# Kernel tuning notes

Measured on AMD Instinct MI355X. Metric: run time of the kernel, lower is better.

## Reference

```python
import jax, jax.numpy as jnp
import numpy as np

N = 100000   # nodes
E = 1600000  # edges
IN_DIM, HID, HEADS, OUT_DIM = 8, 64, 4, 3


def _add_self_loops(src, dst, n):
    loop = jnp.arange(n, dtype=src.dtype)
    return jnp.concatenate([src, loop]), jnp.concatenate([dst, loop])


def gcn_conv(x, src, dst, n, W, b):
    # PyG GCNConv: add self-loops, symmetric normalization deg^-1/2 * deg^-1/2
    s, d = _add_self_loops(src, dst, n)
    deg = jax.ops.segment_sum(jnp.ones(s.shape[0], x.dtype), d, num_segments=n)
    dinv = jnp.where(deg > 0, jax.lax.rsqrt(deg), 0.0)
    norm = dinv[s] * dinv[d]                       # [E']
    h = x @ W                                      # [N, out]
    out = jax.ops.segment_sum(norm[:, None] * h[s], d, num_segments=n)
    return out + b


def gat_conv(x, src, dst, n, W, att_src, att_dst, b):
    # PyG GATConv, concat=True, negative_slope=0.2, self-loops added
    h = (x @ W).reshape(n, HEADS, HID)             # [N, H, C]
    s, d = _add_self_loops(src, dst, n)
    a_src = jnp.sum(h * att_src, axis=-1)          # [N, H]
    a_dst = jnp.sum(h * att_dst, axis=-1)          # [N, H]
    e = jax.nn.leaky_relu(a_src[s] + a_dst[d], negative_slope=0.2)  # [E', H]
    m = jax.lax.stop_gradient(jax.ops.segment_max(e, d, num_segments=n))
    ex = jnp.exp(e - m[d])
    denom = jax.ops.segment_sum(ex, d, num_segments=n)
    alpha = ex / (denom[d] + 1e-16)                # segment softmax over incoming edges
    out = jax.ops.segment_sum(alpha[:, :, None] * h[s], d, num_segments=n)  # [N, H, C]
    return out.reshape(n, HEADS * HID) + b


def setup_inputs() -> dict:
    key = jax.random.key(0)
    ks = jax.random.split(key, 16)
    def glorot(k, shape):
        fan = shape[0] + shape[-1]
        return jax.random.normal(k, shape, jnp.float32) * np.sqrt(2.0 / fan)
    return {
        "x": jax.random.normal(ks[0], (N, IN_DIM), jnp.float32),
        "edge_index": jax.random.randint(ks[1], (2, E), 0, N, jnp.int64 if jax.config.jax_enable_x64 else jnp.int32),
        "w1": glorot(ks[2], (IN_DIM, HID)), "b1": jnp.zeros((HID,), jnp.float32),
        "w2": glorot(ks[3], (HID, HID)),   "b2": jnp.zeros((HID,), jnp.float32),
        "w3": glorot(ks[4], (HID, HID)),   "b3": jnp.zeros((HID,), jnp.float32),
        "wg": glorot(ks[5], (HID, HEADS * HID)), "bg": jnp.zeros((HEADS * HID,), jnp.float32),
        "att_src": glorot(ks[6], (HEADS, HID)),
        "att_dst": glorot(ks[7], (HEADS, HID)),
        "wc1": glorot(ks[8], (HEADS * HID, HID)), "bc1": jnp.zeros((HID,), jnp.float32),
        "wc2": glorot(ks[9], (HID, OUT_DIM)),     "bc2": jnp.zeros((OUT_DIM,), jnp.float32),
    }


def reference(x, edge_index, w1, b1, w2, b2, w3, b3, wg, bg, att_src, att_dst, wc1, bc1, wc2, bc2):
    src, dst = edge_index[0], edge_index[1]
    n = x.shape[0]
    # stacked GCN convs with ReLU; residual when shapes match (layers 2,3)
    h = jax.nn.relu(gcn_conv(x, src, dst, n, w1, b1))
    h = h + jax.nn.relu(gcn_conv(h, src, dst, n, w2, b2))
    h = h + jax.nn.relu(gcn_conv(h, src, dst, n, w3, b3))
    # GAT attention layer (4 heads, concat)
    h_att = gat_conv(h, src, dst, n, wg, att_src, att_dst, bg)  # [N, 256]
    # classifier MLP (dropout is inference no-op)
    z = jax.nn.relu(h_att @ wc1 + bc1)
    logits = z @ wc2 + bc2
    return jax.nn.log_softmax(logits, axis=1)
```

## Files before the change

### kernel.cpp

```cpp
#include <hip/hip_runtime.h>
#include <math.h>


typedef _Float16 half8 __attribute__((ext_vector_type(8)));
typedef _Float16 f16x8 __attribute__((ext_vector_type(8)));
typedef float f32x4 __attribute__((ext_vector_type(4)));

__device__ __forceinline__ float leaky02(float v) { return v > 0.f ? v : 0.2f * v; }


template <int CTRL>
__device__ __forceinline__ float dpp_add(float v) {
    int iv = __builtin_bit_cast(int, v);
    int r = __builtin_amdgcn_update_dpp(iv, iv, CTRL, 0xF, 0xF, false);
    return v + __builtin_bit_cast(float, r);
}
template <int OFF>
__device__ __forceinline__ float swz_add(float v) {
    int r = __builtin_amdgcn_ds_swizzle(__builtin_bit_cast(int, v), OFF);
    return v + __builtin_bit_cast(float, r);
}
__device__ __forceinline__ float red8(float v) {
    v = dpp_add<0xB1>(v);
    v = dpp_add<0x4E>(v);
    v = swz_add<0x101F>(v);
    return v;
}
__device__ __forceinline__ float red16(float v) {
    v = dpp_add<0xB1>(v);
    v = dpp_add<0x4E>(v);
    v = swz_add<0x101F>(v);
    v = dpp_add<0x128>(v);
    return v;
}
__device__ __forceinline__ float red64(float v) {
    v = dpp_add<0xB1>(v);
    v = dpp_add<0x4E>(v);
    v = swz_add<0x101F>(v);
    v = dpp_add<0x128>(v);
    v = swz_add<0x401F>(v);
    v = v + __shfl_xor(v, 32);
    return v;
}
__device__ __forceinline__ float sel4(int g, float v0, float v1, float v2, float v3) {
    return g == 0 ? v0 : g == 1 ? v1 : g == 2 ? v2 : v3;
}


__global__ void count_kernel(const int* __restrict__ dst, int E, int range,
                             int* __restrict__ counts) {
    int grp = blockIdx.x & 7;
    int nlo = grp * range;
    int nhi = nlo + range;
    int nblk = gridDim.x >> 3;
    int c = blockIdx.x >> 3;
    int stride = nblk * blockDim.x;
    for (int e = c * blockDim.x + threadIdx.x; e < E; e += stride) {
        int d = dst[e];
        if (d >= nlo && d < nhi) atomicAdd(&counts[d], 1);
    }
}

__global__ void scan_pass1(const int* __restrict__ counts, int n, int* __restrict__ blockSums) {
    __shared__ int sh[256];
    int base = blockIdx.x * 2048;
    int tid = threadIdx.x;
    int s = 0;
#pragma unroll
    for (int j = 0; j < 8; ++j) {
        int idx = base + tid * 8 + j;
        if (idx < n) s += counts[idx];
    }
    sh[tid] = s;
    __syncthreads();
    for (int off = 128; off > 0; off >>= 1) {
        if (tid < off) sh[tid] += sh[tid + off];
        __syncthreads();
    }
    if (tid == 0) blockSums[blockIdx.x] = sh[0];
}

__global__ void scan_pass2(const int* __restrict__ blockSums, int nb, int* __restrict__ blockOffs) {
    if (threadIdx.x == 0 && blockIdx.x == 0) {
        int run = 0;
        for (int i = 0; i < nb; ++i) { blockOffs[i] = run; run += blockSums[i]; }
    }
}

__global__ void scan_pass3(const int* __restrict__ counts, int n,
                           const int* __restrict__ blockOffs,
                           const float* __restrict__ x,
                           int* __restrict__ row_ptr, int* __restrict__ cursor,
                           float* __restrict__ dinv, float* __restrict__ rdinv,
                           _Float16* __restrict__ xs) {
    __shared__ int sh[256];
    int base = blockIdx.x * 2048;
    int tid = threadIdx.x;
    int cnt[8];
    int local = 0;
#pragma unroll
    for (int j = 0; j < 8; ++j) {
        int idx = base + tid * 8 + j;
        cnt[j] = (idx < n) ? counts[idx] : 0;
        local += cnt[j];
    }
    sh[tid] = local;
    __syncthreads();
    for (int off = 1; off < 256; off <<= 1) {
        int v = (tid >= off) ? sh[tid - off] : 0;
        __syncthreads();
        sh[tid] += v;
        __syncthreads();
    }
    int run = blockOffs[blockIdx.x] + sh[tid] - local;
#pragma unroll
    for (int j = 0; j < 8; ++j) {
        int idx = base + tid * 8 + j;
        if (idx < n) {
            row_ptr[idx] = run;
            cursor[idx] = run;
            float dv = rsqrtf((float)(cnt[j] + 1));
            dinv[idx] = dv;
            rdinv[idx] = sqrtf((float)(cnt[j] + 1));
#pragma unroll
            for (int t = 0; t < 8; ++t) xs[idx * 8 + t] = (_Float16)(dv * x[idx * 8 + t]);
            run += cnt[j];
            if (idx == n - 1) row_ptr[n] = run;
        }
    }
}

__global__ void scatter_kernel(const int* __restrict__ src, const int* __restrict__ dst,
                               int E, int range,
                               int* __restrict__ cursor, int* __restrict__ col_src) {
    int grp = blockIdx.x & 7;
    int nlo = grp * range;
    int nhi = nlo + range;
    int nblk = gridDim.x >> 3;
    int c = blockIdx.x >> 3;
    int stride = nblk * blockDim.x;
    for (int e = c * blockDim.x + threadIdx.x; e < E; e += stride) {
        int d = dst[e];
        if (d >= nlo && d < nhi) {
            int pos = atomicAdd(&cursor[d], 1);
            col_src[pos] = src[e];
        }
    }
}


__global__ void ccomb_kernel(const float* __restrict__ Wg, const float* __restrict__ bg,
                             const float* __restrict__ wc1, const float* __restrict__ bc1,
                             const float* __restrict__ att_src, const float* __restrict__ att_dst,
                             _Float16* __restrict__ CcombP, float* __restrict__ bcomb,
                             float* __restrict__ wse, float* __restrict__ wde) {
    int bid = blockIdx.x;
    int j = threadIdx.x;
    if (bid < 256) {
        int i = bid;
        float s = 0.f;
        for (int c = 0; c < 64; ++c)
            s += Wg[(i & 63) * 256 + (i >> 6) * 64 + c] * wc1[((i >> 6) * 64 + c) * 64 + j];
        _Float16 hi = (_Float16)s;
        _Float16 lo = (_Float16)(s - (float)hi);
        int kt = i >> 5, l = (((i >> 3) & 3) << 4) | (j & 15), e = i & 7, ct = j >> 4;
        CcombP[(ct * 8 + kt) * 512 + l * 8 + e] = hi;
        CcombP[(32 + ct * 8 + kt) * 512 + l * 8 + e] = lo;
    } else {
        float s = bc1[j];
        for (int i = 0; i < 256; ++i) s += bg[i] * wc1[i * 64 + j];
        bcomb[j] = s;
#pragma unroll
        for (int h = 0; h < 4; ++h) {
            float ss = 0.f, sd = 0.f;
            for (int c = 0; c < 64; ++c) {
                float w = Wg[j * 256 + h * 64 + c];
                ss += w * att_src[h * 64 + c];
                sd += w * att_dst[h * 64 + c];
            }
            wse[j * 4 + h] = ss;
            wde[j * 4 + h] = sd;
        }
    }
}


__global__ void gcn_layer1(const half8* __restrict__ xs8,
                           const float* __restrict__ W1, const float* __restrict__ b1,
                           const int* __restrict__ row_ptr, const int* __restrict__ col_src,
                           const float* __restrict__ dinv, int n,
                           _Float16* __restrict__ hs1) {
    int tid = threadIdx.x, lane = tid & 63, wid = tid >> 6;
    int node = blockIdx.x * 4 + wid;
    if (node >= n) return;
    int beg = row_ptr[node], end = row_ptr[node + 1];
    int deg = end - beg;
    float acc[8] = {0.f, 0.f, 0.f, 0.f, 0.f, 0.f, 0.f, 0.f};
    for (int base = 0; base < deg; base += 64) {
        int cs = col_src[min(beg + base + lane, end - 1)];
        half8 v = xs8[cs];
        if (base + lane < deg) {
#pragma unroll
            for (int c = 0; c < 8; ++c) acc[c] += (float)v[c];
        }
    }
#pragma unroll
    for (int c = 0; c < 8; ++c) acc[c] = red64(acc[c]);
    half8 sv = xs8[node];
    float di = dinv[node];
    float agg[8];
#pragma unroll
    for (int c = 0; c < 8; ++c) agg[c] = (acc[c] + (float)sv[c]) * di;
    float sum = b1[lane];
#pragma unroll
    for (int k = 0; k < 8; ++k) sum = fmaf(agg[k], W1[k * 64 + lane], sum);
    hs1[node * 64 + lane] = (_Float16)(di * fmaxf(sum, 0.f));
}


template <bool LAST>
__global__ void gcn_layer64(const _Float16* __restrict__ hs_in,
                            const float* __restrict__ W, const float* __restrict__ b,
                            const int* __restrict__ row_ptr, const int* __restrict__ col_src,
                            const float* __restrict__ dinv, const float* __restrict__ rdinv,
                            const float* __restrict__ wse, const float* __restrict__ wde,
                            int n,
                            _Float16* __restrict__ hout,
                            float4* __restrict__ a_src4, float4* __restrict__ a_dst4) {
    __shared__ float agg_lds[4][64];
    int tid = threadIdx.x;
    int lane = tid & 63;
    int wid = tid >> 6;
    int t = lane >> 3, g = lane & 7;
    const half8* hs8 = (const half8*)hs_in;
    float wreg[64];
#pragma unroll
    for (int k = 0; k < 64; ++k) wreg[k] = W[k * 64 + lane];
    float bl = b[lane];
    float4 we, wd;
    if (LAST) {
        we = ((const float4*)wse)[lane];
        wd = ((const float4*)wde)[lane];
    }
    int nw = gridDim.x * 4;
    for (int node = blockIdx.x * 4 + wid; node < n; node += nw) {
        int beg = row_ptr[node], end = row_ptr[node + 1];
        int deg = end - beg;
        half8 sv = hs8[node * 8 + t];
        float ac[8];
#pragma unroll
        for (int c = 0; c < 8; ++c) ac[c] = (g == 0) ? (float)sv[c] : 0.f;
        for (int base = 0; base < deg; base += 64) {
            int cs = col_src[min(beg + base + lane, end - 1)];
            int lim = min(deg - base, 64);
            auto bodyF = [&](int eo8) {
                int s = __shfl(cs, eo8 + g);
                half8 v = hs8[s * 8 + t];
#pragma unroll
                for (int c = 0; c < 8; ++c) ac[c] += (float)v[c];
            };
            auto bodyG = [&](int eo8) {
                int eo = eo8 + g;
                int s = __shfl(cs, eo);
                half8 v = hs8[s * 8 + t];
                if (eo < lim) {
#pragma unroll
                    for (int c = 0; c < 8; ++c) ac[c] += (float)v[c];
                }
            };
            int eo8 = 0;
            for (; eo8 + 16 <= lim; eo8 += 16) { bodyF(eo8); bodyF(eo8 + 8); }
            if (eo8 < lim) {
                bodyG(eo8);
                eo8 += 8;
                if (eo8 < lim) bodyG(eo8);
            }
        }
        float di = dinv[node];
#pragma unroll
        for (int c = 0; c < 8; ++c) ac[c] = red8(ac[c]) * di;
        if (g == 0) {
            *(float4*)&agg_lds[wid][t * 8]     = make_float4(ac[0], ac[1], ac[2], ac[3]);
            *(float4*)&agg_lds[wid][t * 8 + 4] = make_float4(ac[4], ac[5], ac[6], ac[7]);
        }
        __asm__ volatile("s_waitcnt lgkmcnt(0)" ::: "memory");
        float sum = bl;
#pragma unroll
        for (int k4 = 0; k4 < 16; ++k4) {
            float4 a4 = *(const float4*)&agg_lds[wid][k4 * 4];
            sum = fmaf(a4.x, wreg[k4 * 4 + 0], sum);
            sum = fmaf(a4.y, wreg[k4 * 4 + 1], sum);
            sum = fmaf(a4.z, wreg[k4 * 4 + 2], sum);
            sum = fmaf(a4.w, wreg[k4 * 4 + 3], sum);
        }
        float hprev = rdinv[node] * (float)sv[g];
        float hv = hprev + fmaxf(sum, 0.f);
        if (!LAST) {
            hout[node * 64 + lane] = (_Float16)(di * hv);
        } else {
            hout[node * 64 + lane] = (_Float16)hv;
            float vs0 = red64(hv * we.x), vs1 = red64(hv * we.y);
            float vs2 = red64(hv * we.z), vs3 = red64(hv * we.w);
            float vd0 = red64(hv * wd.x), vd1 = red64(hv * wd.y);
            float vd2 = red64(hv * wd.z), vd3 = red64(hv * wd.w);
            if (lane == 0) {
                a_src4[node] = make_float4(vs0, vs1, vs2, vs3);
                a_dst4[node] = make_float4(vd0, vd1, vd2, vd3);
            }
        }
    }
}


__global__ void gat_agg(const _Float16* __restrict__ h3,
                        const float4* __restrict__ a_src4, const float4* __restrict__ a_dst4,
                        const int* __restrict__ row_ptr, const int* __restrict__ col_src,
                        int n, _Float16* __restrict__ aggout) {
    __shared__ float4 w_lds[4][64];
    __shared__ int    s_lds[4][64];
    int tid = threadIdx.x, lane = tid & 63, wid = tid >> 6;
    int node = blockIdx.x * 4 + wid;
    if (node >= n) return;
    int t = lane >> 3, g = lane & 7;
    const half8* h38 = (const half8*)h3;

    float4 ad = a_dst4[node];
    half8 hself = h38[node * 8 + t];
    float A[4][8], dh[4];
    {
        float4 asf = a_src4[node];
        float w0 = __expf(leaky02(asf.x + ad.x));
        float w1 = __expf(leaky02(asf.y + ad.y));
        float w2 = __expf(leaky02(asf.z + ad.z));
        float w3 = __expf(leaky02(asf.w + ad.w));
        float m0 = (g == 0) ? 1.f : 0.f;
        dh[0] = m0 * w0; dh[1] = m0 * w1; dh[2] = m0 * w2; dh[3] = m0 * w3;
#pragma unroll
        for (int c = 0; c < 8; ++c) {
            float hvc = (float)hself[c];
            A[0][c] = dh[0] * hvc;
            A[1][c] = dh[1] * hvc;
            A[2][c] = dh[2] * hvc;
            A[3][c] = dh[3] * hvc;
        }
    }
    int beg = row_ptr[node], end = row_ptr[node + 1];
    int deg = end - beg;
    for (int base = 0; base < deg; base += 64) {
        int cs = col_src[min(beg + base + lane, end - 1)];
        float4 as = a_src4[cs];
        float valid = (base + lane < deg) ? 1.f : 0.f;
        float4 wv;
        wv.x = valid * __expf(leaky02(as.x + ad.x));
        wv.y = valid * __expf(leaky02(as.y + ad.y));
        wv.z = valid * __expf(leaky02(as.z + ad.z));
        wv.w = valid * __expf(leaky02(as.w + ad.w));
        w_lds[wid][lane] = wv;
        s_lds[wid][lane] = cs;
        __asm__ volatile("s_waitcnt lgkmcnt(0)" ::: "memory");
        int lim = min(deg - base, 64);
        auto body = [&](int eo8) {
            int eo = eo8 + g;
            int s = s_lds[wid][eo];
            float4 w4 = w_lds[wid][eo];
            half8 hv = h38[s * 8 + t];
#pragma unroll
            for (int c = 0; c < 8; ++c) {
                float hvc = (float)hv[c];
                A[0][c] = fmaf(w4.x, hvc, A[0][c]);
                A[1][c] = fmaf(w4.y, hvc, A[1][c]);
                A[2][c] = fmaf(w4.z, hvc, A[2][c]);
                A[3][c] = fmaf(w4.w, hvc, A[3][c]);
            }
            dh[0] += w4.x; dh[1] += w4.y; dh[2] += w4.z; dh[3] += w4.w;
        };
        int eo8 = 0;
        for (; eo8 + 16 <= lim; eo8 += 16) { body(eo8); body(eo8 + 8); }
        if (eo8 < lim) {
            body(eo8);
            eo8 += 8;
            if (eo8 < lim) body(eo8);
        }
    }
#pragma unroll
    for (int h = 0; h < 4; ++h) {
#pragma unroll
        for (int c = 0; c < 8; ++c) A[h][c] = red8(A[h][c]);
        dh[h] = red8(dh[h]);
    }
    float r0 = 1.f / (dh[0] + 1e-16f);
    float r1 = 1.f / (dh[1] + 1e-16f);
    float r2 = 1.f / (dh[2] + 1e-16f);
    float r3 = 1.f / (dh[3] + 1e-16f);
    if (g < 4) {
        float r = sel4(g, r0, r1, r2, r3);
        half8 hv;
#pragma unroll
        for (int c = 0; c < 8; ++c)
            hv[c] = (_Float16)(sel4(g, A[0][c], A[1][c], A[2][c], A[3][c]) * r);
        *(half8*)(aggout + (size_t)node * 256 + g * 64 + t * 8) = hv;
    }
}


__global__ __launch_bounds__(256) void mlp_mfma(
        const _Float16* __restrict__ agg,
        const _Float16* __restrict__ CP,
        const float* __restrict__ bcomb,
        const float* __restrict__ wc2, const float* __restrict__ bc2,
        int n, float* __restrict__ out) {
    __shared__ float part[4][16][3];
    int tid = threadIdx.x;
    int lane = tid & 63;
    int w = __builtin_amdgcn_readfirstlane(tid >> 6);
    int c16 = lane & 15, hi = lane >> 4;

    f16x8 bh[8], blo[8];
#pragma unroll
    for (int kt = 0; kt < 8; ++kt) {
        bh[kt]  = *(const f16x8*)(CP + (size_t)(w * 8 + kt) * 512 + lane * 8);
        blo[kt] = *(const f16x8*)(CP + (size_t)(32 + w * 8 + kt) * 512 + lane * 8);
    }
    int col = w * 16 + c16;
    float bc  = bcomb[col];
    float w20 = wc2[col * 3 + 0], w21 = wc2[col * 3 + 1], w22 = wc2[col * 3 + 2];
    float bb0 = bc2[0], bb1 = bc2[1], bb2 = bc2[2];

    int ntiles = (n + 15) >> 4;
    for (int tile = blockIdx.x; tile < ntiles; tile += gridDim.x) {
        int rowb = tile * 16;
        int row = min(rowb + c16, n - 1);
        const _Float16* ap = agg + (size_t)row * 256 + hi * 8;
        f16x8 a[8];
#pragma unroll
        for (int kt = 0; kt < 8; ++kt) a[kt] = *(const f16x8*)(ap + kt * 32);
        f32x4 acc = {0.f, 0.f, 0.f, 0.f};
#pragma unroll
        for (int kt = 0; kt < 8; ++kt) {
            acc = __builtin_amdgcn_mfma_f32_16x16x32_f16(a[kt], bh[kt],  acc, 0, 0, 0);
            acc = __builtin_amdgcn_mfma_f32_16x16x32_f16(a[kt], blo[kt], acc, 0, 0, 0);
        }
        float pr[4][3];
#pragma unroll
        for (int r = 0; r < 4; ++r) {
            float z = fmaxf(acc[r] + bc, 0.f);
            pr[r][0] = red16(z * w20);
            pr[r][1] = red16(z * w21);
            pr[r][2] = red16(z * w22);
        }
        if (c16 == 0) {
#pragma unroll
            for (int r = 0; r < 4; ++r) {
                part[w][hi * 4 + r][0] = pr[r][0];
                part[w][hi * 4 + r][1] = pr[r][1];
                part[w][hi * 4 + r][2] = pr[r][2];
            }
        }
        __syncthreads();
        if (tid < 16) {
            int node = rowb + tid;
            if (node < n) {
                float e0 = part[0][tid][0] + part[1][tid][0] + part[2][tid][0] + part[3][tid][0] + bb0;
                float e1 = part[0][tid][1] + part[1][tid][1] + part[2][tid][1] + part[3][tid][1] + bb1;
                float e2 = part[0][tid][2] + part[1][tid][2] + part[2][tid][2] + part[3][tid][2] + bb2;
                float mx = fmaxf(e0, fmaxf(e1, e2));
                float lse = mx + logf(expf(e0 - mx) + expf(e1 - mx) + expf(e2 - mx));
                out[(size_t)node * 3 + 0] = e0 - lse;
                out[(size_t)node * 3 + 1] = e1 - lse;
                out[(size_t)node * 3 + 2] = e2 - lse;
            }
        }
        __syncthreads();
    }
}


extern "C" void kernel_launch(void* const* d_in, const int* in_sizes, int n_in,
                              void* d_out, int out_size, void* d_ws, size_t ws_size,
                              hipStream_t stream) {
    const float* x       = (const float*)d_in[0];
    const int*   ei      = (const int*)d_in[1];
    const float* w1      = (const float*)d_in[2];
    const float* b1      = (const float*)d_in[3];
    const float* w2      = (const float*)d_in[4];
    const float* b2      = (const float*)d_in[5];
    const float* w3      = (const float*)d_in[6];
    const float* b3      = (const float*)d_in[7];
    const float* wg      = (const float*)d_in[8];
    const float* bg      = (const float*)d_in[9];
    const float* att_s   = (const float*)d_in[10];
    const float* att_d   = (const float*)d_in[11];
    const float* wc1     = (const float*)d_in[12];
    const float* bc1     = (const float*)d_in[13];
    const float* wc2     = (const float*)d_in[14];
    const float* bc2     = (const float*)d_in[15];
    float* out = (float*)d_out;

    const int N = in_sizes[0] / 8;
    const int E = in_sizes[1] / 2;
    const int* srcv = ei;
    const int* dstv = ei + E;

    char* ws = (char*)d_ws;
    size_t off = 0;
    auto alloc = [&](size_t bytes) -> char* {
        char* p = ws + off;
        off += (bytes + 255) & ~(size_t)255;
        return p;
    };
    int*      counts    = (int*)alloc((size_t)N * 4);
    int*      row_ptr   = (int*)alloc((size_t)(N + 1) * 4);
    int*      cursor    = (int*)alloc((size_t)N * 4);
    int*      col_src   = (int*)alloc((size_t)E * 4);
    int*      blockSums = (int*)alloc(4096 * 4);
    int*      blockOffs = (int*)alloc(4096 * 4);
    float*    dinv      = (float*)alloc((size_t)N * 4);
    float*    rdinv     = (float*)alloc((size_t)N * 4);
    _Float16* xs        = (_Float16*)alloc((size_t)N * 8 * 2);
    float*    a_src     = (float*)alloc((size_t)N * 16);
    float*    a_dst     = (float*)alloc((size_t)N * 16);
    float*    wse       = (float*)alloc(256 * 4);
    float*    wde       = (float*)alloc(256 * 4);
    _Float16* CcombP    = (_Float16*)alloc(64 * 1024);
    float*    bcomb     = (float*)alloc(64 * 4);
    _Float16* bufA      = (_Float16*)alloc((size_t)N * 64 * 2);
    _Float16* bufB      = (_Float16*)alloc((size_t)N * 64 * 2);
    _Float16* aggbuf    = (_Float16*)alloc((size_t)N * 256 * 2);
    _Float16* hs1 = bufA;
    _Float16* hs2 = bufB;
    _Float16* h3  = bufA;
    (void)ws_size; (void)n_in; (void)out_size;

    hipMemsetAsync(counts, 0, (size_t)N * 4, stream);

    const int TPB = 256;
    int range = (N + 7) / 8;
    count_kernel<<<1024, TPB, 0, stream>>>(dstv, E, range, counts);

    int NB = (N + 2047) / 2048;
    scan_pass1<<<NB, TPB, 0, stream>>>(counts, N, blockSums);
    scan_pass2<<<1, 64, 0, stream>>>(blockSums, NB, blockOffs);
    scan_pass3<<<NB, TPB, 0, stream>>>(counts, N, blockOffs, x,
                                       row_ptr, cursor, dinv, rdinv, xs);
    scatter_kernel<<<2048, TPB, 0, stream>>>(srcv, dstv, E, range, cursor, col_src);

    ccomb_kernel<<<257, 64, 0, stream>>>(wg, bg, wc1, bc1, att_s, att_d,
                                         CcombP, bcomb, wse, wde);

    int gridN = (N + 3) / 4;
    gcn_layer1<<<gridN, TPB, 0, stream>>>((const half8*)xs, w1, b1, row_ptr, col_src,
                                          dinv, N, hs1);
    const int G64 = 2048;
    gcn_layer64<false><<<G64, TPB, 0, stream>>>(hs1, w2, b2, row_ptr, col_src,
                                                dinv, rdinv, wse, wde, N, hs2,
                                                nullptr, nullptr);
    gcn_layer64<true><<<G64, TPB, 0, stream>>>(hs2, w3, b3, row_ptr, col_src,
                                               dinv, rdinv, wse, wde, N, h3,
                                               (float4*)a_src, (float4*)a_dst);

    gat_agg<<<gridN, TPB, 0, stream>>>(h3, (const float4*)a_src, (const float4*)a_dst,
                                       row_ptr, col_src, N, aggbuf);
    mlp_mfma<<<2048, TPB, 0, stream>>>(aggbuf, CcombP, bcomb, wc2, bc2, N, out);
}
```

Baseline: 560.4 us.

## Compute GAT neighbor aggregation with MFMA over LDS-staged neighbor features

Replaces the per-lane scalar FMA aggregation in gat_agg with 16x16x32 fp16 MFMA. Each chunk of up to 32 incoming edges, with the self-loop as slot 0, is staged into LDS along with the attention weights. Weights are split into fp16 hi/lo parts so the products keep more precision, and the per-node max from the first chunk is subtracted before exp, with the exponent clamped at 10. This targets the VALU cost of the 4-head weighted sum, but adds LDS staging traffic, wasted MFMA rows for low-degree nodes, and numerical changes from the clamp.

```diff
diff --git a/kernel.cpp b/kernel.cpp
--- a/kernel.cpp
+++ b/kernel.cpp
@@ -19,6 +19,17 @@
 __device__ __forceinline__ float swz_add(float v) {
     int r = __builtin_amdgcn_ds_swizzle(__builtin_bit_cast(int, v), OFF);
     return v + __builtin_bit_cast(float, r);
+}
+template <int CTRL>
+__device__ __forceinline__ float dpp_max(float v) {
+    int iv = __builtin_bit_cast(int, v);
+    int r = __builtin_amdgcn_update_dpp(iv, iv, CTRL, 0xF, 0xF, false);
+    return fmaxf(v, __builtin_bit_cast(float, r));
+}
+template <int OFF>
+__device__ __forceinline__ float swz_max(float v) {
+    int r = __builtin_amdgcn_ds_swizzle(__builtin_bit_cast(int, v), OFF);
+    return fmaxf(v, __builtin_bit_cast(float, r));
 }
 __device__ __forceinline__ float red8(float v) {
     v = dpp_add<0xB1>(v);
@@ -42,8 +53,14 @@
     v = v + __shfl_xor(v, 32);
     return v;
 }
-__device__ __forceinline__ float sel4(int g, float v0, float v1, float v2, float v3) {
-    return g == 0 ? v0 : g == 1 ? v1 : g == 2 ? v2 : v3;
+__device__ __forceinline__ float red64max(float v) {
+    v = dpp_max<0xB1>(v);
+    v = dpp_max<0x4E>(v);
+    v = swz_max<0x101F>(v);
+    v = dpp_max<0x128>(v);
+    v = swz_max<0x401F>(v);
+    v = fmaxf(v, __shfl_xor(v, 32));
+    return v;
 }
 
 
@@ -316,89 +333,108 @@
                         const float4* __restrict__ a_src4, const float4* __restrict__ a_dst4,
                         const int* __restrict__ row_ptr, const int* __restrict__ col_src,
                         int n, _Float16* __restrict__ aggout) {
-    __shared__ float4 w_lds[4][64];
-    __shared__ int    s_lds[4][64];
+    __shared__ _Float16 HsAll[4][32 * 72];
+    __shared__ _Float16 wATAll[4][16 * 40];
     int tid = threadIdx.x, lane = tid & 63, wid = tid >> 6;
     int node = blockIdx.x * 4 + wid;
     if (node >= n) return;
-    int t = lane >> 3, g = lane & 7;
-    const half8* h38 = (const half8*)h3;
-
+    _Float16* Hs = HsAll[wid];
+    _Float16* wAT = wATAll[wid];
+
+    int q = lane >> 4, m16 = lane & 15;
     float4 ad = a_dst4[node];
-    half8 hself = h38[node * 8 + t];
-    float A[4][8], dh[4];
-    {
-        float4 asf = a_src4[node];
-        float w0 = __expf(leaky02(asf.x + ad.x));
-        float w1 = __expf(leaky02(asf.y + ad.y));
-        float w2 = __expf(leaky02(asf.z + ad.z));
-        float w3 = __expf(leaky02(asf.w + ad.w));
-        float m0 = (g == 0) ? 1.f : 0.f;
-        dh[0] = m0 * w0; dh[1] = m0 * w1; dh[2] = m0 * w2; dh[3] = m0 * w3;
-#pragma unroll
-        for (int c = 0; c < 8; ++c) {
-            float hvc = (float)hself[c];
-            A[0][c] = dh[0] * hvc;
-            A[1][c] = dh[1] * hvc;
-            A[2][c] = dh[2] * hvc;
-            A[3][c] = dh[3] * hvc;
-        }
-    }
     int beg = row_ptr[node], end = row_ptr[node + 1];
     int deg = end - beg;
-    for (int base = 0; base < deg; base += 64) {
-        int cs = col_src[min(beg + base + lane, end - 1)];
+    int nslots = deg + 1;
+
+    f32x4 acc0 = {0.f,0.f,0.f,0.f}, acc1 = {0.f,0.f,0.f,0.f};
+    f32x4 acc2 = {0.f,0.f,0.f,0.f}, acc3 = {0.f,0.f,0.f,0.f};
+    float dh0 = 0.f, dh1 = 0.f, dh2 = 0.f, dh3 = 0.f;
+    float m0 = 0.f, m1 = 0.f, m2 = 0.f, m3 = 0.f;
+    int c0 = (lane & 7) * 8;
+
+    for (int base = 0; base < nslots; base += 32) {
+        int sl = base + (lane & 31);
+        int eidx = max(min(beg + sl - 1, end - 1), 0);
+        int cs = (sl == 0) ? node : col_src[eidx];
         float4 as = a_src4[cs];
-        float valid = (base + lane < deg) ? 1.f : 0.f;
-        float4 wv;
-        wv.x = valid * __expf(leaky02(as.x + ad.x));
-        wv.y = valid * __expf(leaky02(as.y + ad.y));
-        wv.z = valid * __expf(leaky02(as.z + ad.z));
-        wv.w = valid * __expf(leaky02(as.w + ad.w));
-        w_lds[wid][lane] = wv;
-        s_lds[wid][lane] = cs;
+        float vm = (sl < nslots && lane < 32) ? 1.f : 0.f;
+        float l0 = leaky02(as.x + ad.x);
+        float l1 = leaky02(as.y + ad.y);
+        float l2 = leaky02(as.z + ad.z);
+        float l3 = leaky02(as.w + ad.w);
+        if (base == 0) {
+            m0 = red64max(vm > 0.f ? l0 : -1e30f);
+            m1 = red64max(vm > 0.f ? l1 : -1e30f);
+            m2 = red64max(vm > 0.f ? l2 : -1e30f);
+            m3 = red64max(vm > 0.f ? l3 : -1e30f);
+        }
+        float w0 = vm * __expf(fminf(l0 - m0, 10.f));
+        float w1 = vm * __expf(fminf(l1 - m1, 10.f));
+        float w2 = vm * __expf(fminf(l2 - m2, 10.f));
+        float w3 = vm * __expf(fminf(l3 - m3, 10.f));
+        dh0 += w0; dh1 += w1; dh2 += w2; dh3 += w3;
+        if (lane < 32) {
+            int s32 = lane & 31;
+            _Float16 h0 = (_Float16)w0, h1 = (_Float16)w1;
+            _Float16 h2 = (_Float16)w2, h3v = (_Float16)w3;
+            wAT[0 * 40 + s32] = h0;
+            wAT[1 * 40 + s32] = h1;
+            wAT[2 * 40 + s32] = h2;
+            wAT[3 * 40 + s32] = h3v;
+            wAT[4 * 40 + s32] = (_Float16)(w0 - (float)h0);
+            wAT[5 * 40 + s32] = (_Float16)(w1 - (float)h1);
+            wAT[6 * 40 + s32] = (_Float16)(w2 - (float)h2);
+            wAT[7 * 40 + s32] = (_Float16)(w3 - (float)h3v);
+        }
+#pragma unroll
+        for (int i = 0; i < 4; ++i) {
+            int r = i * 8 + (lane >> 3);
+            int s = __shfl(cs, r);
+            half8 hv = *(const half8*)(h3 + (size_t)s * 64 + c0);
+            *(half8*)(Hs + r * 72 + (c0 ^ (i << 4))) = hv;
+        }
         __asm__ volatile("s_waitcnt lgkmcnt(0)" ::: "memory");
-        int lim = min(deg - base, 64);
-        auto body = [&](int eo8) {
-            int eo = eo8 + g;
-            int s = s_lds[wid][eo];
-            float4 w4 = w_lds[wid][eo];
-            half8 hv = h38[s * 8 + t];
-#pragma unroll
-            for (int c = 0; c < 8; ++c) {
-                float hvc = (float)hv[c];
-                A[0][c] = fmaf(w4.x, hvc, A[0][c]);
-                A[1][c] = fmaf(w4.y, hvc, A[1][c]);
-                A[2][c] = fmaf(w4.z, hvc, A[2][c]);
-                A[3][c] = fmaf(w4.w, hvc, A[3][c]);
-            }
-            dh[0] += w4.x; dh[1] += w4.y; dh[2] += w4.z; dh[3] += w4.w;
-        };
-        int eo8 = 0;
-        for (; eo8 + 16 <= lim; eo8 += 16) { body(eo8); body(eo8 + 8); }
-        if (eo8 < lim) {
-            body(eo8);
-            eo8 += 8;
-            if (eo8 < lim) body(eo8);
-        }
-    }
-#pragma unroll
-    for (int h = 0; h < 4; ++h) {
-#pragma unroll
-        for (int c = 0; c < 8; ++c) A[h][c] = red8(A[h][c]);
-        dh[h] = red8(dh[h]);
-    }
-    float r0 = 1.f / (dh[0] + 1e-16f);
-    float r1 = 1.f / (dh[1] + 1e-16f);
-    float r2 = 1.f / (dh[2] + 1e-16f);
-    float r3 = 1.f / (dh[3] + 1e-16f);
-    if (g < 4) {
-        float r = sel4(g, r0, r1, r2, r3);
-        half8 hv;
-#pragma unroll
-        for (int c = 0; c < 8; ++c)
-            hv[c] = (_Float16)(sel4(g, A[0][c], A[1][c], A[2][c], A[3][c]) * r);
-        *(half8*)(aggout + (size_t)node * 256 + g * 64 + t * 8) = hv;
+        f16x8 A = *(const f16x8*)(wAT + m16 * 40 + q * 8);
+        f16x8 B0, B1, B2, B3;
+#pragma unroll
+        for (int e = 0; e < 8; ++e) {
+            int k = q * 8 + e;
+            int rb = k * 72;
+            B0[e] = Hs[rb + ((0 * 16 + m16) ^ (q << 4))];
+            B1[e] = Hs[rb + ((1 * 16 + m16) ^ (q << 4))];
+            B2[e] = Hs[rb + ((2 * 16 + m16) ^ (q << 4))];
+            B3[e] = Hs[rb + ((3 * 16 + m16) ^ (q << 4))];
+        }
+        acc0 = __builtin_amdgcn_mfma_f32_16x16x32_f16(A, B0, acc0, 0, 0, 0);
+        acc1 = __builtin_amdgcn_mfma_f32_16x16x32_f16(A, B1, acc1, 0, 0, 0);
+        acc2 = __builtin_amdgcn_mfma_f32_16x16x32_f16(A, B2, acc2, 0, 0, 0);
+        acc3 = __builtin_amdgcn_mfma_f32_16x16x32_f16(A, B3, acc3, 0, 0, 0);
+        __asm__ volatile("s_waitcnt lgkmcnt(0)" ::: "memory");
+    }
+
+    dh0 = red64(dh0); dh1 = red64(dh1); dh2 = red64(dh2); dh3 = red64(dh3);
+    float rd[4];
+    rd[0] = 1.f / (dh0 + 1e-16f);
+    rd[1] = 1.f / (dh1 + 1e-16f);
+    rd[2] = 1.f / (dh2 + 1e-16f);
+    rd[3] = 1.f / (dh3 + 1e-16f);
+    float tot[4][4];
+#pragma unroll
+    for (int r = 0; r < 4; ++r) {
+        tot[0][r] = acc0[r] + __shfl_xor(acc0[r], 16);
+        tot[1][r] = acc1[r] + __shfl_xor(acc1[r], 16);
+        tot[2][r] = acc2[r] + __shfl_xor(acc2[r], 16);
+        tot[3][r] = acc3[r] + __shfl_xor(acc3[r], 16);
+    }
+    if (lane < 16) {
+        size_t ob = (size_t)node * 256 + lane;
+#pragma unroll
+        for (int r = 0; r < 4; ++r) {
+#pragma unroll
+            for (int ct = 0; ct < 4; ++ct)
+                aggout[ob + r * 64 + ct * 16] = (_Float16)(tot[ct][r] * rd[r]);
+        }
     }
 }
 
```

Result: no change. 551.7 us (-1.6%).
